# Kernel optimization log

Measured on AMD Instinct MI355X. Metric: run time of the kernel, lower is better.

The kernel has to match this reference:

```python
import jax, jax.numpy as jnp
import numpy as np

EPS = 1e-12  # F.normalize default eps


def _l2_normalize(v):
    # torch.nn.functional.normalize(v, dim=1): v / max(||v||_2, eps)
    n = jnp.sqrt(jnp.sum(v * v, axis=1, keepdims=True))
    return v / jnp.maximum(n, EPS)


def _max_cut_grad(x, src, dst, edge_weight, num_nodes):
    # MessagePassing(aggr='add'): message = x_j * w, scatter-add at dst
    msg = x[src] * edge_weight[:, None]          # [E, r]
    return jax.ops.segment_sum(msg, dst, num_segments=num_nodes)  # [N, r]


def setup_inputs() -> dict:
    key = jax.random.key(0)
    ks = jax.random.split(key, 8)
    N, E, r = 50000, 1600000, 32
    L_lift, L_proj = 8, 4
    x = jax.random.normal(ks[0], (N, r), dtype=jnp.float32)
    edge_index = jax.random.randint(ks[1], (2, E), 0, N, dtype=jnp.int64)
    edge_weight = jax.random.normal(ks[2], (E,), dtype=jnp.float32)
    s = 1.0 / np.sqrt(2 * r)
    lift_W = jax.random.uniform(ks[3], (L_lift, 2 * r, r), jnp.float32, -s, s)
    lift_b = jax.random.uniform(ks[4], (L_lift, r), jnp.float32, -s, s)
    proj_W = jax.random.uniform(ks[5], (L_proj, 2 * r, r), jnp.float32, -s, s)
    proj_b = jax.random.uniform(ks[6], (L_proj, r), jnp.float32, -s, s)
    return {"x": x, "edge_index": edge_index, "edge_weight": edge_weight,
            "lift_W": lift_W, "lift_b": lift_b, "proj_W": proj_W, "proj_b": proj_b}


def reference(x, edge_index, edge_weight, lift_W, lift_b, proj_W, proj_b):
    N = x.shape[0]
    src, dst = edge_index[0], edge_index[1]

    # Lift layers: grads -> normalize -> concat -> Linear -> normalize
    def lift_step(h, wb):
        W, b = wb
        g = _l2_normalize(_max_cut_grad(h, src, dst, edge_weight, N))
        out = jnp.concatenate([h, g], axis=1) @ W + b
        return _l2_normalize(out), None

    x, _ = jax.lax.scan(lift_step, x, (lift_W, lift_b))

    # Project layers: grads -> concat -> Linear -> tanh
    def proj_step(h, wb):
        W, b = wb
        g = _max_cut_grad(h, src, dst, edge_weight, N)
        out = jnp.concatenate([h, g], axis=1) @ W + b
        return jnp.tanh(out), None

    x, _ = jax.lax.scan(proj_step, x, (proj_W, proj_b))
    return x
```

## Files before the change

kernel.cpp:

```cpp
#include <hip/hip_runtime.h>
#include <hip/hip_fp16.h>
#include <math.h>


#define R 32
#define EPSN 1e-12f
#define BINW 256
#define CAP  9216
#define EPB  4096
#define NPB  16
#define GSTR 16

typedef unsigned short u16;
typedef unsigned int   u32;

__device__ __forceinline__ u16 f2h(float f) {
    return __half_as_ushort(__float2half_rn(f));
}

__launch_bounds__(1024)
__global__ void bin_scatter_kernel(const int* __restrict__ ei, const float* __restrict__ ew,
                                   int* __restrict__ gcur, int2* __restrict__ binned,
                                   int E, int nb) {
    __shared__ int lhist[BINW];
    __shared__ int lbase[BINW];
    __shared__ int lcur[BINW];
    const int tid = threadIdx.x;
    for (int i = tid; i < nb; i += 1024) { lhist[i] = 0; lcur[i] = 0; }
    __syncthreads();
    const int e0 = blockIdx.x * EPB;
    const int e1 = min(e0 + EPB, E);

    int dv[4], sv[4]; float wv[4];
    #pragma unroll
    for (int k = 0; k < 4; ++k) {
        const int e = e0 + tid + k * 1024;
        const bool ok = (e < e1);
        dv[k] = ok ? ei[E + e] : -1;
        sv[k] = ok ? ei[e] : 0;
        wv[k] = ok ? ew[e] : 0.f;
    }
    #pragma unroll
    for (int k = 0; k < 4; ++k)
        if (dv[k] >= 0) atomicAdd(&lhist[dv[k] >> 8], 1);
    __syncthreads();
    for (int i = tid; i < nb; i += 1024)
        lbase[i] = atomicAdd(&gcur[i * GSTR], lhist[i]);
    __syncthreads();
    #pragma unroll
    for (int k = 0; k < 4; ++k) {
        if (dv[k] < 0) continue;
        const int bin = dv[k] >> 8, dl = dv[k] & 255;
        const int slot = lbase[bin] + atomicAdd(&lcur[bin], 1);
        if (slot < CAP)
            binned[(size_t)bin * CAP + slot] = make_int2(sv[k] | (dl << 16), __float_as_int(wv[k]));
    }
}

__global__ void bin_scan_kernel(const int* __restrict__ gcur, int* __restrict__ binoff, int nb) {
    __shared__ int s[256];
    const int tid = threadIdx.x;
    const int v0 = (tid < nb) ? gcur[tid * GSTR] : 0;
    s[tid] = v0;
    __syncthreads();
    for (int off = 1; off < 256; off <<= 1) {
        int v = (tid >= off) ? s[tid - off] : 0;
        __syncthreads();
        s[tid] += v;
        __syncthreads();
    }
    if (tid < nb) binoff[tid] = s[tid] - v0;
}

__launch_bounds__(256)
__global__ void csr_build_kernel(const int2* __restrict__ binned, const int* __restrict__ gcur,
                                 const int* __restrict__ binoff,
                                 int* __restrict__ offsets, int2* __restrict__ csr,
                                 int N, int E, int nb) {
    __shared__ int cnt[BINW];
    __shared__ int sc[BINW];
    __shared__ int excl[BINW];
    __shared__ int cur[BINW];
    const int b = blockIdx.x;
    const int tid = threadIdx.x;
    cnt[tid] = 0; cur[tid] = 0;
    __syncthreads();
    const int2* src = binned + (size_t)b * CAP;
    const int n = gcur[b * GSTR];
    const int base = binoff[b];
    for (int i = tid; i < n; i += 256)
        atomicAdd(&cnt[((unsigned)src[i].x) >> 16], 1);
    __syncthreads();
    sc[tid] = cnt[tid];
    __syncthreads();
    for (int off = 1; off < 256; off <<= 1) {
        int v = (tid >= off) ? sc[tid - off] : 0;
        __syncthreads();
        sc[tid] += v;
        __syncthreads();
    }
    excl[tid] = sc[tid] - cnt[tid];
    const int node = b * BINW + tid;
    if (node < N) offsets[node] = base + excl[tid];
    if (b == nb - 1 && tid == 0) offsets[N] = E;
    __syncthreads();
    for (int i = tid; i < n; i += 256) {
        const int2 p = src[i];
        const unsigned key = (unsigned)p.x;
        const int dl = key >> 16;
        const int s  = key & 0xffff;
        const int slot = base + excl[dl] + atomicAdd(&cur[dl], 1);
        csr[slot] = make_int2(s << 6, p.y);
    }
}

__global__ void transpose_W_kernel(const float* __restrict__ liftW,
                                   const float* __restrict__ projW,
                                   float* __restrict__ WT) {
    const int l = blockIdx.x;
    const float* W = (l < 8) ? liftW + (size_t)l * 2048 : projW + (size_t)(l - 8) * 2048;
    float* T = WT + (size_t)l * 2048;
    for (int i = threadIdx.x; i < 2048; i += 256) {
        const int k = i >> 5, j = i & 31;
        T[j * 64 + k] = W[i];
    }
}

__global__ void cvt_x_kernel(const float* __restrict__ x, u16* __restrict__ xH, int total8) {
    const int t = blockIdx.x * 256 + threadIdx.x;
    if (t >= total8) return;
    const float4 v0 = reinterpret_cast<const float4*>(x)[t * 2];
    const float4 v1 = reinterpret_cast<const float4*>(x)[t * 2 + 1];
    u16 o[8] = { f2h(v0.x), f2h(v0.y), f2h(v0.z), f2h(v0.w),
                 f2h(v1.x), f2h(v1.y), f2h(v1.z), f2h(v1.w) };
    reinterpret_cast<uint4*>(xH)[t] = *reinterpret_cast<uint4*>(o);
}

template <bool LIFT, bool FINAL>
__launch_bounds__(512, 8)
__global__ void layer_kernel(const u16*  __restrict__ hH,
                             const int*  __restrict__ offsets,
                             const int2* __restrict__ csr,
                             const float* __restrict__ WT,
                             const float* __restrict__ bias,
                             u16*  __restrict__ outH,
                             float* __restrict__ outF,
                             int N) {
    __shared__ float WsT[32][68];
    __shared__ float hg[NPB][64];

    const int tid = threadIdx.x;
    {
        const float4 v = *reinterpret_cast<const float4*>(WT + tid * 4);
        *reinterpret_cast<float4*>(&WsT[tid >> 4][(tid & 15) * 4]) = v;
    }
    __syncthreads();

    const int grp   = tid >> 5;
    const int j     = tid & 31;
    const int sub   = j & 3;
    const int eslot = j >> 2;
    const unsigned fo = (unsigned)sub * 16u;
    const int node  = blockIdx.x * NPB + grp;
    const char* hb  = (const char*)hH;

    hg[grp][j] = __half2float(((const __half*)hH)[(size_t)node * R + j]);

    const int beg = offsets[node];
    const int end = offsets[node + 1];
    float a0=0.f,a1=0.f,a2=0.f,a3=0.f,a4=0.f,a5=0.f,a6=0.f,a7=0.f;
    {
        const int  p0 = (end > beg) ? min(beg + j, end - 1) : 0;
        int2 q = csr[p0];
        int   oj = q.x;
        float wj = (beg + j < end) ? __int_as_float(q.y) : 0.f;

        for (int base = beg; base < end; base += 32) {
            const int  np = min(base + 32 + j, end - 1);
            const int2 qn = csr[np];
            const int   on = qn.x;
            const float wn = (base + 32 + j < end) ? __int_as_float(qn.y) : 0.f;

            #pragma unroll
            for (int s = 0; s < 4; ++s) {
                const int   sl  = s * 8 + eslot;
                const int   off = __shfl(oj, sl, 32);
                const float w   = __shfl(wj, sl, 32);
                const uint4 hv  = *reinterpret_cast<const uint4*>(hb + (unsigned)off + fo);
                const float2 f01 = __half22float2(*reinterpret_cast<const __half2*>(&hv.x));
                const float2 f23 = __half22float2(*reinterpret_cast<const __half2*>(&hv.y));
                const float2 f45 = __half22float2(*reinterpret_cast<const __half2*>(&hv.z));
                const float2 f67 = __half22float2(*reinterpret_cast<const __half2*>(&hv.w));
                a0 = fmaf(f01.x, w, a0); a1 = fmaf(f01.y, w, a1);
                a2 = fmaf(f23.x, w, a2); a3 = fmaf(f23.y, w, a3);
                a4 = fmaf(f45.x, w, a4); a5 = fmaf(f45.y, w, a5);
                a6 = fmaf(f67.x, w, a6); a7 = fmaf(f67.y, w, a7);
            }
            oj = on; wj = wn;
        }
    }
    #pragma unroll
    for (int m = 4; m <= 16; m <<= 1) {
        a0 += __shfl_xor(a0, m, 32); a1 += __shfl_xor(a1, m, 32);
        a2 += __shfl_xor(a2, m, 32); a3 += __shfl_xor(a3, m, 32);
        a4 += __shfl_xor(a4, m, 32); a5 += __shfl_xor(a5, m, 32);
        a6 += __shfl_xor(a6, m, 32); a7 += __shfl_xor(a7, m, 32);
    }

    if (LIFT) {
        float ss = a0*a0 + a1*a1 + a2*a2 + a3*a3 + a4*a4 + a5*a5 + a6*a6 + a7*a7;
        ss += __shfl_xor(ss, 1, 32);
        ss += __shfl_xor(ss, 2, 32);
        const float sc = 1.f / fmaxf(sqrtf(ss), EPSN);
        a0 *= sc; a1 *= sc; a2 *= sc; a3 *= sc;
        a4 *= sc; a5 *= sc; a6 *= sc; a7 *= sc;
    }
    if (j < 4) {
        *reinterpret_cast<float4*>(&hg[grp][32 + j * 8])     = make_float4(a0, a1, a2, a3);
        *reinterpret_cast<float4*>(&hg[grp][32 + j * 8 + 4]) = make_float4(a4, a5, a6, a7);
    }

    float acc0 = bias[j], acc1 = 0.f;
    #pragma unroll
    for (int kb = 0; kb < 16; ++kb) {
        const float4 r  = *reinterpret_cast<const float4*>(&hg[grp][kb * 4]);
        const float4 wv = *reinterpret_cast<const float4*>(&WsT[j][kb * 4]);
        float& acc = (kb & 1) ? acc1 : acc0;
        acc = fmaf(r.x, wv.x, acc);
        acc = fmaf(r.y, wv.y, acc);
        acc = fmaf(r.z, wv.z, acc);
        acc = fmaf(r.w, wv.w, acc);
    }
    float acc = acc0 + acc1;

    if (LIFT) {
        float s = acc * acc;
        #pragma unroll
        for (int o = 16; o >= 1; o >>= 1) s += __shfl_xor(s, o, 32);
        acc = acc / fmaxf(sqrtf(s), EPSN);
    } else {
        acc = tanhf(acc);
    }

    if (FINAL)
        outF[(size_t)node * R + j] = acc;
    else
        outH[(size_t)node * R + j] = f2h(acc);
}

extern "C" void kernel_launch(void* const* d_in, const int* in_sizes, int n_in,
                              void* d_out, int out_size, void* d_ws, size_t ws_size,
                              hipStream_t stream) {
    const float* x      = (const float*)d_in[0];
    const int*   ei     = (const int*)d_in[1];
    const float* ew     = (const float*)d_in[2];
    const float* lift_W = (const float*)d_in[3];
    const float* lift_b = (const float*)d_in[4];
    const float* proj_W = (const float*)d_in[5];
    const float* proj_b = (const float*)d_in[6];

    const int N = in_sizes[0] / R;
    const int E = in_sizes[2];
    const int nb = (N + BINW - 1) / BINW;

    int*   offsets = (int*)d_ws;
    int*   gcur    = offsets + N + 1;
    int*   binoff  = gcur + 256 * GSTR;
    float* WT      = (float*)(binoff + 256);
    uintptr_t p    = (uintptr_t)(WT + 12 * 2048);
    p = (p + 15) & ~(uintptr_t)15;
    int2*  binned  = (int2*)p;
    int2*  csr     = binned + (size_t)nb * CAP;
    u16*   xH      = (u16*)binned;
    u16*   hHa     = xH  + (size_t)N * R;
    u16*   hHb     = hHa + (size_t)N * R;

    hipMemsetAsync(gcur, 0, 256 * GSTR * sizeof(int), stream);
    transpose_W_kernel<<<12, 256, 0, stream>>>(lift_W, proj_W, WT);
    bin_scatter_kernel<<<(E + EPB - 1) / EPB, 1024, 0, stream>>>(ei, ew, gcur, binned, E, nb);
    bin_scan_kernel<<<1, 256, 0, stream>>>(gcur, binoff, nb);
    csr_build_kernel<<<nb, 256, 0, stream>>>(binned, gcur, binoff, offsets, csr, N, E, nb);
    const int total8 = N * R / 8;
    cvt_x_kernel<<<(total8 + 255) / 256, 256, 0, stream>>>(x, xH, total8);

    const u16* curH = xH;
    float* fout = (float*)d_out;
    const int node_blocks = N / NPB;

    for (int l = 0; l < 12; ++l) {
        const float* Wc = WT + (size_t)l * 2048;
        const float* b  = (l < 8) ? (lift_b + (size_t)l * R) : (proj_b + (size_t)(l - 8) * R);
        u16* dstH = (l & 1) ? hHb : hHa;
        if (l < 8)
            layer_kernel<true , false><<<node_blocks, 512, 0, stream>>>(curH, offsets, csr, Wc, b, dstH, nullptr, N);
        else if (l < 11)
            layer_kernel<false, false><<<node_blocks, 512, 0, stream>>>(curH, offsets, csr, Wc, b, dstH, nullptr, N);
        else
            layer_kernel<false, true ><<<node_blocks, 512, 0, stream>>>(curH, offsets, csr, Wc, b, nullptr, fout, N);
        curH = dstH;
    }
}
```

Before: 424.2 us.

## Pack CSR edges into 32-bit fp16-weight words and sort nodes by degree bucket

Each CSR entry shrinks from an int2 (byte offset plus fp32 weight) to one 32-bit word holding a 16-bit source index and an fp16 edge weight. This halves the edge-stream traffic read in every one of the twelve layers. It also adds a degree-bucket permutation built by two new small kernels, so each block processes nodes of similar degree and warp-group loop trip counts are balanced. The costs are reduced weight precision, a 65535-node limit on source indices, extra setup kernels, and scattered output writes through the permutation.

After: 406.4 us, median of 2. 1.04x faster.

```diff
diff --git a/kernel.cpp b/kernel.cpp
--- a/kernel.cpp
+++ b/kernel.cpp
@@ -75,15 +75,18 @@
 __launch_bounds__(256)
 __global__ void csr_build_kernel(const int2* __restrict__ binned, const int* __restrict__ gcur,
                                  const int* __restrict__ binoff,
-                                 int* __restrict__ offsets, int2* __restrict__ csr,
+                                 int* __restrict__ offsets, u32* __restrict__ csrp,
+                                 int* __restrict__ bucket_cnt,
                                  int N, int E, int nb) {
     __shared__ int cnt[BINW];
     __shared__ int sc[BINW];
     __shared__ int excl[BINW];
     __shared__ int cur[BINW];
+    __shared__ int bc8[8];
     const int b = blockIdx.x;
     const int tid = threadIdx.x;
     cnt[tid] = 0; cur[tid] = 0;
+    if (tid < 8) bc8[tid] = 0;
     __syncthreads();
     const int2* src = binned + (size_t)b * CAP;
     const int n = gcur[b * GSTR];
@@ -101,16 +104,50 @@
     }
     excl[tid] = sc[tid] - cnt[tid];
     const int node = b * BINW + tid;
-    if (node < N) offsets[node] = base + excl[tid];
+    if (node < N) {
+        offsets[node] = base + excl[tid];
+        atomicAdd(&bc8[min(7, (cnt[tid] + 31) >> 5)], 1);
+    }
     if (b == nb - 1 && tid == 0) offsets[N] = E;
     __syncthreads();
+    if (tid < 8 && bc8[tid] > 0) atomicAdd(&bucket_cnt[tid * GSTR], bc8[tid]);
     for (int i = tid; i < n; i += 256) {
         const int2 p = src[i];
         const unsigned key = (unsigned)p.x;
         const int dl = key >> 16;
-        const int s  = key & 0xffff;
+        const u32 s  = key & 0xffffu;
         const int slot = base + excl[dl] + atomicAdd(&cur[dl], 1);
-        csr[slot] = make_int2(s << 6, p.y);
+        csrp[slot] = ((u32)f2h(__int_as_float(p.y)) << 16) | s;
+    }
+}
+
+__global__ void bucket_scan_kernel(const int* __restrict__ bucket_cnt, int* __restrict__ bcur) {
+    if (threadIdx.x == 0) {
+        int run = 0;
+        for (int i = 0; i < 8; ++i) { bcur[i * GSTR] = run; run += bucket_cnt[i * GSTR]; }
+    }
+}
+
+__launch_bounds__(256)
+__global__ void perm_fill_kernel(const int* __restrict__ offsets, int* __restrict__ bcur,
+                                 int* __restrict__ perm, int N) {
+    __shared__ int cnt8[8], base8[8], idx8[8];
+    const int tid = threadIdx.x;
+    const int node = blockIdx.x * 256 + tid;
+    if (tid < 8) { cnt8[tid] = 0; idx8[tid] = 0; }
+    __syncthreads();
+    int wc = 0;
+    if (node < N) {
+        const int d = offsets[node + 1] - offsets[node];
+        wc = min(7, (d + 31) >> 5);
+        atomicAdd(&cnt8[wc], 1);
+    }
+    __syncthreads();
+    if (tid < 8 && cnt8[tid] > 0) base8[tid] = atomicAdd(&bcur[tid * GSTR], cnt8[tid]);
+    __syncthreads();
+    if (node < N) {
+        const int p = base8[wc] + atomicAdd(&idx8[wc], 1);
+        perm[p] = node;
     }
 }
 
@@ -140,7 +177,8 @@
 __launch_bounds__(512, 8)
 __global__ void layer_kernel(const u16*  __restrict__ hH,
                              const int*  __restrict__ offsets,
-                             const int2* __restrict__ csr,
+                             const u32*  __restrict__ csrp,
+                             const int*  __restrict__ perm,
                              const float* __restrict__ WT,
                              const float* __restrict__ bias,
                              u16*  __restrict__ outH,
@@ -161,7 +199,7 @@
     const int sub   = j & 3;
     const int eslot = j >> 2;
     const unsigned fo = (unsigned)sub * 16u;
-    const int node  = blockIdx.x * NPB + grp;
+    const int node  = perm[blockIdx.x * NPB + grp];
     const char* hb  = (const char*)hH;
 
     hg[grp][j] = __half2float(((const __half*)hH)[(size_t)node * R + j]);
@@ -169,24 +207,19 @@
     const int beg = offsets[node];
     const int end = offsets[node + 1];
     float a0=0.f,a1=0.f,a2=0.f,a3=0.f,a4=0.f,a5=0.f,a6=0.f,a7=0.f;
-    {
-        const int  p0 = (end > beg) ? min(beg + j, end - 1) : 0;
-        int2 q = csr[p0];
-        int   oj = q.x;
-        float wj = (beg + j < end) ? __int_as_float(q.y) : 0.f;
+    if (end > beg) {
+        u32 q = csrp[min(beg + j, end - 1)];
+        if (beg + j >= end) q &= 0xffffu;
 
         for (int base = beg; base < end; base += 32) {
-            const int  np = min(base + 32 + j, end - 1);
-            const int2 qn = csr[np];
-            const int   on = qn.x;
-            const float wn = (base + 32 + j < end) ? __int_as_float(qn.y) : 0.f;
+            u32 qn = csrp[min(base + 32 + j, end - 1)];
+            if (base + 32 + j >= end) qn &= 0xffffu;
 
             #pragma unroll
             for (int s = 0; s < 4; ++s) {
-                const int   sl  = s * 8 + eslot;
-                const int   off = __shfl(oj, sl, 32);
-                const float w   = __shfl(wj, sl, 32);
-                const uint4 hv  = *reinterpret_cast<const uint4*>(hb + (unsigned)off + fo);
+                const u32  qq = (u32)__shfl((int)q, s * 8 + eslot, 32);
+                const float w = __half2float(__ushort_as_half((u16)(qq >> 16)));
+                const uint4 hv = *reinterpret_cast<const uint4*>(hb + ((qq & 0xffffu) << 6) + fo);
                 const float2 f01 = __half22float2(*reinterpret_cast<const __half2*>(&hv.x));
                 const float2 f23 = __half22float2(*reinterpret_cast<const __half2*>(&hv.y));
                 const float2 f45 = __half22float2(*reinterpret_cast<const __half2*>(&hv.z));
@@ -196,7 +229,7 @@
                 a4 = fmaf(f45.x, w, a4); a5 = fmaf(f45.y, w, a5);
                 a6 = fmaf(f67.x, w, a6); a7 = fmaf(f67.y, w, a7);
             }
-            oj = on; wj = wn;
+            q = qn;
         }
     }
     #pragma unroll
@@ -266,20 +299,26 @@
     int*   offsets = (int*)d_ws;
     int*   gcur    = offsets + N + 1;
     int*   binoff  = gcur + 256 * GSTR;
-    float* WT      = (float*)(binoff + 256);
+    int*   bcnt    = binoff + 256;
+    int*   bcur    = bcnt + 8 * GSTR;
+    int*   perm    = bcur + 8 * GSTR;
+    float* WT      = (float*)(perm + N);
     uintptr_t p    = (uintptr_t)(WT + 12 * 2048);
     p = (p + 15) & ~(uintptr_t)15;
     int2*  binned  = (int2*)p;
-    int2*  csr     = binned + (size_t)nb * CAP;
+    u32*   csrp    = (u32*)(binned + (size_t)nb * CAP);
     u16*   xH      = (u16*)binned;
     u16*   hHa     = xH  + (size_t)N * R;
     u16*   hHb     = hHa + (size_t)N * R;
 
-    hipMemsetAsync(gcur, 0, 256 * GSTR * sizeof(int), stream);
+    const size_t ctr_ints = 256 * GSTR + 256 + 8 * GSTR + 8 * GSTR;
+    hipMemsetAsync(gcur, 0, ctr_ints * sizeof(int), stream);
     transpose_W_kernel<<<12, 256, 0, stream>>>(lift_W, proj_W, WT);
     bin_scatter_kernel<<<(E + EPB - 1) / EPB, 1024, 0, stream>>>(ei, ew, gcur, binned, E, nb);
     bin_scan_kernel<<<1, 256, 0, stream>>>(gcur, binoff, nb);
-    csr_build_kernel<<<nb, 256, 0, stream>>>(binned, gcur, binoff, offsets, csr, N, E, nb);
+    csr_build_kernel<<<nb, 256, 0, stream>>>(binned, gcur, binoff, offsets, csrp, bcnt, N, E, nb);
+    bucket_scan_kernel<<<1, 64, 0, stream>>>(bcnt, bcur);
+    perm_fill_kernel<<<nb, 256, 0, stream>>>(offsets, bcur, perm, N);
     const int total8 = N * R / 8;
     cvt_x_kernel<<<(total8 + 255) / 256, 256, 0, stream>>>(x, xH, total8);
 
@@ -292,11 +331,11 @@
         const float* b  = (l < 8) ? (lift_b + (size_t)l * R) : (proj_b + (size_t)(l - 8) * R);
         u16* dstH = (l & 1) ? hHb : hHa;
         if (l < 8)
-            layer_kernel<true , false><<<node_blocks, 512, 0, stream>>>(curH, offsets, csr, Wc, b, dstH, nullptr, N);
+            layer_kernel<true , false><<<node_blocks, 512, 0, stream>>>(curH, offsets, csrp, perm, Wc, b, dstH, nullptr, N);
         else if (l < 11)
-            layer_kernel<false, false><<<node_blocks, 512, 0, stream>>>(curH, offsets, csr, Wc, b, dstH, nullptr, N);
+            layer_kernel<false, false><<<node_blocks, 512, 0, stream>>>(curH, offsets, csrp, perm, Wc, b, dstH, nullptr, N);
         else
-            layer_kernel<false, true ><<<node_blocks, 512, 0, stream>>>(curH, offsets, csr, Wc, b, nullptr, fout, N);
+            layer_kernel<false, true ><<<node_blocks, 512, 0, stream>>>(curH, offsets, csrp, perm, Wc, b, nullptr, fout, N);
         curH = dstH;
     }
 }
```
